# Kernel tuning notes

Hardware: AMD Instinct MI355X
Metric: run time of the kernel (lower is better)

The kernel has to match this reference:

```python
import jax, jax.numpy as jnp
import numpy as np

HID = 1024
HEADS = 16
HEAD_DIM = HID // HEADS
MAX_P = 64
TAB = 2 * MAX_P + 1
B, L = 8, 512


def setup_inputs() -> dict:
    key = jax.random.key(0)
    ks = jax.random.split(key, 16)
    def lin(k, fan_in, fan_out):
        lim = 1.0 / np.sqrt(fan_in)
        kw, kb = jax.random.split(k)
        W = jax.random.uniform(kw, (fan_out, fan_in), jnp.float32, -lim, lim)
        b = jax.random.uniform(kb, (fan_out,), jnp.float32, -lim, lim)
        return W, b
    Wq, bq = lin(ks[0], HID, HID)
    Wk, bk = lin(ks[1], HID, HID)
    Wv, bv = lin(ks[2], HID, HID)
    Wo, bo = lin(ks[3], HID, HID)
    # xavier_uniform for relative-position tables
    xlim = float(np.sqrt(6.0 / (TAB + HEAD_DIM)))
    table_k = jax.random.uniform(ks[4], (TAB, HEAD_DIM), jnp.float32, -xlim, xlim)
    table_v = jax.random.uniform(ks[5], (TAB, HEAD_DIM), jnp.float32, -xlim, xlim)
    return {
        "query": jax.random.normal(ks[6], (B, L, HID), jnp.float32),
        "key": jax.random.normal(ks[7], (B, L, HID), jnp.float32),
        "value": jax.random.normal(ks[8], (B, L, HID), jnp.float32),
        "final_mat": jax.random.randint(ks[9], (B, L, L), 0, TAB, jnp.int64 if jax.config.jax_enable_x64 else jnp.int32),
        "Wq": Wq, "bq": bq, "Wk": Wk, "bk": bk,
        "Wv": Wv, "bv": bv, "Wo": Wo, "bo": bo,
        "table_k": table_k, "table_v": table_v,
    }


def reference(query, key, value, final_mat, Wq, bq, Wk, bk, Wv, bv, Wo, bo, table_k, table_v):
    Bt, Lq, D = query.shape
    H, hd = HEADS, HEAD_DIM
    q = query @ Wq.T + bq          # [B,Lq,D]
    k = key @ Wk.T + bk            # [B,Lk,D]
    v = value @ Wv.T + bv          # [B,Lv,D]
    q4 = q.reshape(Bt, Lq, H, hd)
    k4 = k.reshape(Bt, -1, H, hd)
    v4 = v.reshape(Bt, -1, H, hd)
    # content-content scores
    attn1 = jnp.einsum('bqhd,bkhd->bhqk', q4, k4)
    # content-position scores via gathered relative-key embeddings [B,Lq,Lk,hd]
    rk = table_k[final_mat]
    attn2 = jnp.einsum('bqhd,bqkd->bhqk', q4, rk)
    scale = jnp.asarray(np.sqrt(hd), q.dtype)
    attn = jax.nn.softmax((attn1 + attn2) / scale, axis=-1)  # [B,H,Lq,Lk]
    # dropout p=0 (eval)
    w1 = jnp.einsum('bhqk,bkhd->bqhd', attn, v4)
    rv = table_v[final_mat]                                   # [B,Lq,Lk,hd]
    w2 = jnp.einsum('bhqk,bqkd->bqhd', attn, rv)
    x = (w1 + w2).reshape(Bt, Lq, D)
    return x @ Wo.T + bo
```

## Files before the change

kernel.cpp:

```cpp
#include <hip/hip_runtime.h>

#define HID 1024
#define HEADS 16
#define HD 64
#define TAB 129
#define QSTR 136
#define BATCH 8
#define SEQ 512

typedef unsigned int uint;
typedef unsigned short ushort;
typedef unsigned char uchar;
typedef __attribute__((ext_vector_type(4))) float f32x4;
typedef __attribute__((ext_vector_type(8))) __bf16 bf16x8;

__device__ __forceinline__ ushort f2b(float x) {
    uint b = __float_as_uint(x);
    uint r = (b + 0x7fffu + ((b >> 16) & 1u)) >> 16;
    return (ushort)r;
}
__device__ __forceinline__ uint pk(float lo, float hi) {
    return (uint)f2b(lo) | ((uint)f2b(hi) << 16);
}
__device__ __forceinline__ float b2f(ushort u) {
    return __uint_as_float(((uint)u) << 16);
}
union U16x8 { uint u[4]; bf16x8 v; ushort s[8]; uint4 q; };

#define GL16(gp, lp) __builtin_amdgcn_global_load_lds( \
    (const __attribute__((address_space(1))) void*)(gp), \
    (__attribute__((address_space(3))) void*)(lp), 16, 0, 0)

struct ConvArgs { const float* src[7]; ushort* dst[7]; };

__global__ __launch_bounds__(256) void convert_bf16(ConvArgs ca) {
    int bid = blockIdx.x;
    int ti, lb;
    if (bid < 6144) { ti = bid >> 11; lb = bid & 2047; }
    else { int r = bid - 6144; ti = 3 + (r >> 9); lb = r & 511; }
    const float* s = ca.src[ti] + (size_t)lb * 2048 + (threadIdx.x << 3);
    ushort*      d = ca.dst[ti] + (size_t)lb * 2048 + (threadIdx.x << 3);
    float4 a = *(const float4*)s;
    float4 c = *(const float4*)(s + 4);
    uint4 u;
    u.x = pk(a.x, a.y); u.y = pk(a.z, a.w);
    u.z = pk(c.x, c.y); u.w = pk(c.z, c.w);
    *(uint4*)d = u;
}

struct GemmArgs {
    const ushort* A[3];
    const ushort* W[3];
    const float*  bias[3];
    ushort*       Cb[3];
};

__global__ __launch_bounds__(256) void gemm_qkv(GemmArgs ga) {
    const int N = HID, K = HID;
    __shared__ ushort As[2][128 * 32];
    __shared__ ushort Bs[2][64 * 32];
    const int tid = threadIdx.x;
    const int bid = blockIdx.x;
    const int swz = (bid & 7) * 192 + (bid >> 3);
    const int z   = swz >> 9;
    const int rem = swz & 511;
    const int m0  = (rem >> 4) * 128;
    const int n0  = (rem & 15) * 64;
    const ushort* A = ga.A[z];
    const ushort* W = ga.W[z];

    const int w  = tid >> 6;
    const int l  = tid & 63;
    const int lr = l & 15;
    const int lg = l >> 4;
    const int wm = w >> 1;
    const int wn = w & 1;

    const int sr = tid >> 2;
    const int sc = tid & 3;
    const int g  = sc ^ ((sr >> 1) & 3);
    const ushort* Ag0 = A + (size_t)(m0 + sr)      * K + g * 8;
    const ushort* Ag1 = A + (size_t)(m0 + sr + 64) * K + g * 8;
    const ushort* Wg0 = W + (size_t)(n0 + sr)      * K + g * 8;

    f32x4 acc[4][2];
#pragma unroll
    for (int mt = 0; mt < 4; ++mt)
#pragma unroll
        for (int nt = 0; nt < 2; ++nt) acc[mt][nt] = (f32x4){0.f, 0.f, 0.f, 0.f};

#define STAGE(buf, k0) do { \
        GL16(Ag0 + (k0), &As[buf][w * 512]); \
        GL16(Ag1 + (k0), &As[buf][2048 + w * 512]); \
        GL16(Wg0 + (k0), &Bs[buf][w * 512]); \
    } while (0)

    const int swl = (lr >> 1) & 3;
#define COMPUTE(buf) do { \
        bf16x8 af[4], bf[2]; \
        _Pragma("unroll") \
        for (int mt = 0; mt < 4; ++mt) \
            af[mt] = *(const bf16x8*)&As[buf][(wm * 64 + mt * 16 + lr) * 32 + (lg ^ swl) * 8]; \
        _Pragma("unroll") \
        for (int nt = 0; nt < 2; ++nt) \
            bf[nt] = *(const bf16x8*)&Bs[buf][(wn * 32 + nt * 16 + lr) * 32 + (lg ^ swl) * 8]; \
        _Pragma("unroll") \
        for (int mt = 0; mt < 4; ++mt) \
            _Pragma("unroll") \
            for (int nt = 0; nt < 2; ++nt) \
                acc[mt][nt] = __builtin_amdgcn_mfma_f32_16x16x32_bf16(af[mt], bf[nt], acc[mt][nt], 0, 0, 0); \
    } while (0)

    STAGE(0, 0);
    __syncthreads();
    const int nk = K / 32;
    for (int t = 0; t < nk - 1; ++t) {
        STAGE((t + 1) & 1, (size_t)(t + 1) * 32);
        COMPUTE(t & 1);
        __syncthreads();
    }
    COMPUTE((nk - 1) & 1);

    const float* bias = ga.bias[z];
    float bv[2];
#pragma unroll
    for (int nt = 0; nt < 2; ++nt) bv[nt] = bias[n0 + wn * 32 + nt * 16 + lr];
    ushort* Cb = ga.Cb[z];
#pragma unroll
    for (int mt = 0; mt < 4; ++mt)
#pragma unroll
        for (int r4 = 0; r4 < 4; ++r4) {
            size_t m = m0 + wm * 64 + mt * 16 + lg * 4 + r4;
            ushort* crow = Cb + m * N + n0 + wn * 32 + lr;
#pragma unroll
            for (int nt = 0; nt < 2; ++nt)
                crow[nt * 16] = f2b(acc[mt][nt][r4] + bv[nt]);
        }
#undef STAGE
#undef COMPUTE
}

__global__ __launch_bounds__(256) void gemm_wo(const ushort* __restrict__ A,
                                               const ushort* __restrict__ W,
                                               const float* __restrict__ bias,
                                               float* __restrict__ Cf) {
    const int M = BATCH * SEQ, N = HID, K = HID;
    __shared__ ushort As[2][128 * 32];
    __shared__ ushort Bs[2][64 * 32];
    const int tid = threadIdx.x;
    const int m0 = blockIdx.y * 128;
    const int n0 = blockIdx.x * 64;

    const int w  = tid >> 6;
    const int l  = tid & 63;
    const int lr = l & 15;
    const int lg = l >> 4;
    const int wm = w >> 1;
    const int wn = w & 1;

    const int sr = tid >> 2;
    const int sc = tid & 3;
    const int g  = sc ^ ((sr >> 1) & 3);
    const ushort* Ag0 = A + (size_t)(m0 + sr)      * K + g * 8;
    const ushort* Ag1 = A + (size_t)(m0 + sr + 64) * K + g * 8;
    const ushort* Wg0 = W + (size_t)(n0 + sr)      * K + g * 8;

    f32x4 acc[4][2];
#pragma unroll
    for (int mt = 0; mt < 4; ++mt)
#pragma unroll
        for (int nt = 0; nt < 2; ++nt) acc[mt][nt] = (f32x4){0.f, 0.f, 0.f, 0.f};

#define STAGE(buf, k0) do { \
        GL16(Ag0 + (k0), &As[buf][w * 512]); \
        GL16(Ag1 + (k0), &As[buf][2048 + w * 512]); \
        GL16(Wg0 + (k0), &Bs[buf][w * 512]); \
    } while (0)

    const int swl = (lr >> 1) & 3;
#define COMPUTE(buf) do { \
        bf16x8 af[4], bf[2]; \
        _Pragma("unroll") \
        for (int mt = 0; mt < 4; ++mt) \
            af[mt] = *(const bf16x8*)&As[buf][(wm * 64 + mt * 16 + lr) * 32 + (lg ^ swl) * 8]; \
        _Pragma("unroll") \
        for (int nt = 0; nt < 2; ++nt) \
            bf[nt] = *(const bf16x8*)&Bs[buf][(wn * 32 + nt * 16 + lr) * 32 + (lg ^ swl) * 8]; \
        _Pragma("unroll") \
        for (int mt = 0; mt < 4; ++mt) \
            _Pragma("unroll") \
            for (int nt = 0; nt < 2; ++nt) \
                acc[mt][nt] = __builtin_amdgcn_mfma_f32_16x16x32_bf16(af[mt], bf[nt], acc[mt][nt], 0, 0, 0); \
    } while (0)

    STAGE(0, 0);
    __syncthreads();
    const int nk = K / 32;
    for (int t = 0; t < nk - 1; ++t) {
        STAGE((t + 1) & 1, (size_t)(t + 1) * 32);
        COMPUTE(t & 1);
        __syncthreads();
    }
    COMPUTE((nk - 1) & 1);

    float bv[2];
#pragma unroll
    for (int nt = 0; nt < 2; ++nt) bv[nt] = bias[n0 + wn * 32 + nt * 16 + lr];
#pragma unroll
    for (int mt = 0; mt < 4; ++mt)
#pragma unroll
        for (int r4 = 0; r4 < 4; ++r4) {
            size_t m = m0 + wm * 64 + mt * 16 + lg * 4 + r4;
            float* crow = Cf + m * N + n0 + wn * 32 + lr;
#pragma unroll
            for (int nt = 0; nt < 2; ++nt)
                crow[nt * 16] = acc[mt][nt][r4] + bv[nt];
        }
#undef STAGE
#undef COMPUTE
}

__global__ __launch_bounds__(256) void prep_kernel(const ushort* __restrict__ qb,
                                                   const float* __restrict__ table_k,
                                                   const ushort* __restrict__ vb,
                                                   const float* __restrict__ table_v,
                                                   const int* __restrict__ fmat,
                                                   ushort* __restrict__ qtab,
                                                   ushort* __restrict__ vT,
                                                   ushort* __restrict__ tvT2,
                                                   uchar* __restrict__ fm8) {
    __shared__ __align__(16) ushort shmem[144 * 72];
    const int wg  = blockIdx.x;
    const int tid = threadIdx.x;

    if (wg < 256) {
        const int h    = wg & 15;
        const int half = (wg >> 4) & 1;
        const int b    = wg >> 5;
        const int q0   = half * 256;
        ushort* tk = shmem;
        for (int i = tid; i < TAB * 8; i += 256) {
            int row = i >> 3, gr = i & 7;
            const float* src = table_k + row * HD + gr * 8;
            float4 a = *(const float4*)src;
            float4 c = *(const float4*)(src + 4);
            uint4 u;
            u.x = pk(a.x, a.y); u.y = pk(a.z, a.w);
            u.z = pk(c.x, c.y); u.w = pk(c.z, c.w);
            *(uint4*)&tk[row * 72 + gr * 8] = u;
        }
        __syncthreads();

        const int w  = tid >> 6;
        const int l  = tid & 63;
        const int lr = l & 15;
        const int lg = l >> 4;
        bf16x8 qf[4][2];
#pragma unroll
        for (int qt = 0; qt < 4; ++qt) {
            const ushort* qrow = qb + ((size_t)(b * SEQ) + q0 + w * 64 + qt * 16 + lr) * HID + h * HD;
            qf[qt][0] = *(const bf16x8*)(qrow + lg * 8);
            qf[qt][1] = *(const bf16x8*)(qrow + 32 + lg * 8);
        }
        ushort* outbase = qtab + ((size_t)(b * HEADS + h) * SEQ + q0 + w * 64) * QSTR;
#pragma unroll
        for (int mt = 0; mt < 9; ++mt) {
            bf16x8 tf0 = *(const bf16x8*)&tk[(mt * 16 + lr) * 72 + lg * 8];
            bf16x8 tf1 = *(const bf16x8*)&tk[(mt * 16 + lr) * 72 + 32 + lg * 8];
#pragma unroll
            for (int qt = 0; qt < 4; ++qt) {
                f32x4 acc = (f32x4){0.f, 0.f, 0.f, 0.f};
                acc = __builtin_amdgcn_mfma_f32_16x16x32_bf16(tf0, qf[qt][0], acc, 0, 0, 0);
                acc = __builtin_amdgcn_mfma_f32_16x16x32_bf16(tf1, qf[qt][1], acc, 0, 0, 0);
                ushort* orow = outbase + (size_t)(qt * 16 + lr) * QSTR;
                if (mt < 8) {
                    uint2 pu;
                    pu.x = pk(acc[0], acc[1]); pu.y = pk(acc[2], acc[3]);
                    *(uint2*)&orow[mt * 16 + lg * 4] = pu;
                } else if (lg == 0) {
                    orow[128] = f2b(acc[0]);
                }
            }
        }
    } else if (wg < 768) {
        const int vw = wg - 256;
        ushort* tile = shmem;
        const int b = vw >> 6, h = (vw >> 2) & 15, kc = vw & 3;
        const int k0 = kc * 128;
        {
            const int kr = tid >> 1, dc = (tid & 1) * 32;
            const ushort* src = vb + ((size_t)(b * SEQ) + k0 + kr) * HID + h * 64 + dc;
#pragma unroll
            for (int j = 0; j < 4; ++j) {
                uint4 u = *(const uint4*)(src + j * 8);
                *(uint4*)&tile[kr * 72 + dc + j * 8] = u;
            }
        }
        __syncthreads();
        {
            const int dr = tid >> 2, kc2 = (tid & 3) * 32;
            ushort* dst = vT + ((size_t)(b * 16 + h) * 64 + dr) * 512 + k0 + kc2;
#pragma unroll
            for (int j = 0; j < 4; ++j) {
                U16x8 o;
#pragma unroll
                for (int i = 0; i < 8; ++i)
                    o.s[i] = tile[(kc2 + j * 8 + i) * 72 + dr];
                *(uint4*)(dst + j * 8) = o.q;
            }
        }
    } else if (wg == 768) {
        for (int i = tid; i < 64 * 160; i += 256) {
            int d = i / 160;
            int c = i - d * 160;
            tvT2[i] = (c < TAB) ? f2b(table_v[(size_t)c * HD + d]) : (ushort)0;
        }
    } else {
        const size_t base = (size_t)(wg - 769) * 2048 + (size_t)tid * 8;
        int4 a = *(const int4*)(fmat + base);
        int4 c = *(const int4*)(fmat + base + 4);
        uint lo = (uint)a.x | ((uint)a.y << 8) | ((uint)a.z << 16) | ((uint)a.w << 24);
        uint hi = (uint)c.x | ((uint)c.y << 8) | ((uint)c.z << 16) | ((uint)c.w << 24);
        uint2 o; o.x = lo; o.y = hi;
        *(uint2*)(fm8 + base) = o;
    }
}

__global__ __launch_bounds__(256) void qk_gemm(const ushort* __restrict__ qb,
                                               const ushort* __restrict__ kb,
                                               ushort* __restrict__ S) {
    __shared__ ushort As[2][128 * 32];
    __shared__ ushort Bs[2][128 * 32];
    const int tid = threadIdx.x;
    const int m0 = blockIdx.x * 128;
    const int n0 = blockIdx.y * 128;
    const int bh = blockIdx.z;
    const int b = bh >> 4, h = bh & 15;
    const size_t rowQ = (size_t)b * SEQ;

    const int w  = tid >> 6;
    const int l  = tid & 63;
    const int lr = l & 15;
    const int lg = l >> 4;
    const int wm = w >> 1;
    const int wn = w & 1;

    const int sr = tid >> 2;
    const int sc = tid & 3;
    const int g  = sc ^ ((sr >> 1) & 3);
    const ushort* Ag0 = qb + (rowQ + m0 + sr)      * HID + h * HD + g * 8;
    const ushort* Ag1 = qb + (rowQ + m0 + sr + 64) * HID + h * HD + g * 8;
    const ushort* Wg0 = kb + (rowQ + n0 + sr)      * HID + h * HD + g * 8;
    const ushort* Wg1 = kb + (rowQ + n0 + sr + 64) * HID + h * HD + g * 8;

    GL16(Ag0,      &As[0][w * 512]); GL16(Ag1,      &As[0][2048 + w * 512]);
    GL16(Wg0,      &Bs[0][w * 512]); GL16(Wg1,      &Bs[0][2048 + w * 512]);
    GL16(Ag0 + 32, &As[1][w * 512]); GL16(Ag1 + 32, &As[1][2048 + w * 512]);
    GL16(Wg0 + 32, &Bs[1][w * 512]); GL16(Wg1 + 32, &Bs[1][2048 + w * 512]);

    f32x4 acc[4][4];
#pragma unroll
    for (int mt = 0; mt < 4; ++mt)
#pragma unroll
        for (int nt = 0; nt < 4; ++nt) acc[mt][nt] = (f32x4){0.f, 0.f, 0.f, 0.f};

    const int swl = (lr >> 1) & 3;
    __syncthreads();
#pragma unroll
    for (int buf = 0; buf < 2; ++buf) {
        bf16x8 af[4], bf[4];
#pragma unroll
        for (int mt = 0; mt < 4; ++mt)
            af[mt] = *(const bf16x8*)&As[buf][(wm * 64 + mt * 16 + lr) * 32 + (lg ^ swl) * 8];
#pragma unroll
        for (int nt = 0; nt < 4; ++nt)
            bf[nt] = *(const bf16x8*)&Bs[buf][(wn * 64 + nt * 16 + lr) * 32 + (lg ^ swl) * 8];
#pragma unroll
        for (int mt = 0; mt < 4; ++mt)
#pragma unroll
            for (int nt = 0; nt < 4; ++nt)
                acc[mt][nt] = __builtin_amdgcn_mfma_f32_16x16x32_bf16(af[mt], bf[nt], acc[mt][nt], 0, 0, 0);
    }

    ushort* Sb = S + (size_t)bh * SEQ * SEQ;
#pragma unroll
    for (int mt = 0; mt < 4; ++mt)
#pragma unroll
        for (int r4 = 0; r4 < 4; ++r4) {
            int m = m0 + wm * 64 + mt * 16 + lg * 4 + r4;
            ushort* srow = Sb + (size_t)m * SEQ + n0 + wn * 64 + lr;
#pragma unroll
            for (int nt = 0; nt < 4; ++nt)
                srow[nt * 16] = f2b(acc[mt][nt][r4]);
        }
}

__global__ __launch_bounds__(256) void sm_kernel(ushort* __restrict__ S,
                                                 const ushort* __restrict__ qt,
                                                 const uchar* __restrict__ fm8,
                                                 ushort* __restrict__ binbuf) {
    constexpr float FIX = 65536.0f;
    constexpr float INV_FIX = 1.0f / 65536.0f;
    __shared__ uint binsL[4][160];
    const int tid = threadIdx.x;
    const int wv  = tid >> 6;
    const int l   = tid & 63;
    const int gr0 = blockIdx.x * 32 + wv * 8;

    for (int ri = 0; ri < 8; ++ri) {
        const int gr = gr0 + ri;
        const int q  = gr & 511;
        const int b  = gr >> 13;
        binsL[wv][l] = 0u;
        binsL[wv][l + 64] = 0u;
        if (l < 32) binsL[wv][l + 128] = 0u;

        U16x8 sv;
        sv.q = *(const uint4*)&S[((size_t)gr << 9) + l * 8];
        const uchar* fr = fm8 + ((((size_t)b << 9) + q) << 9) + l * 8;
        uint f0 = *(const uint*)fr;
        uint f1 = *(const uint*)(fr + 4);
        const ushort* qrow = qt + (size_t)gr * QSTR;

        int ts[8];
        ts[0] = f0 & 255; ts[1] = (f0 >> 8) & 255; ts[2] = (f0 >> 16) & 255; ts[3] = f0 >> 24;
        ts[4] = f1 & 255; ts[5] = (f1 >> 8) & 255; ts[6] = (f1 >> 16) & 255; ts[7] = f1 >> 24;

        float pr[8];
        float lsum = 0.f;
#pragma unroll
        for (int j = 0; j < 8; ++j) {
            float s = b2f(sv.s[j]);
            float gv = b2f(qrow[ts[j]]);
            pr[j] = __expf((s + gv) * 0.125f);
            lsum += pr[j];
        }
#pragma unroll
        for (int j = 0; j < 8; ++j)
            __hip_atomic_fetch_add(&binsL[wv][ts[j]], (uint)(pr[j] * FIX),
                                   __ATOMIC_RELAXED, __HIP_MEMORY_SCOPE_WORKGROUP);
#pragma unroll
        for (int off = 32; off >= 1; off >>= 1)
            lsum += __shfl_xor(lsum, off);
        const float invl = 1.f / lsum;

        U16x8 pv;
#pragma unroll
        for (int j = 0; j < 4; ++j)
            pv.u[j] = pk(pr[2 * j] * invl, pr[2 * j + 1] * invl);
        *(uint4*)&S[((size_t)gr << 9) + l * 8] = pv.q;

        asm volatile("s_waitcnt lgkmcnt(0)" ::: "memory");
        ushort* bb = binbuf + (size_t)gr * 160;
        const float sc = INV_FIX * invl;
        {
            int c = 2 * l;
            *(uint*)&bb[c] = pk((float)binsL[wv][c] * sc, (float)binsL[wv][c + 1] * sc);
        }
        if (l < 16) {
            int c = 128 + 2 * l;
            *(uint*)&bb[c] = pk((float)binsL[wv][c] * sc, (float)binsL[wv][c + 1] * sc);
        }
    }
}

__global__ __launch_bounds__(256) void pv_gemm(const ushort* __restrict__ P,
                                               const ushort* __restrict__ binbuf,
                                               const ushort* __restrict__ vT,
                                               const ushort* __restrict__ tvT2,
                                               ushort* __restrict__ x) {
    __shared__ ushort As[2][128 * 32];
    __shared__ ushort Bs[2][64 * 32];
    const int tid = threadIdx.x;
    const int m0 = blockIdx.x * 128;
    const int bh = blockIdx.y;
    const int b = bh >> 4, h = bh & 15;

    const int w  = tid >> 6;
    const int l  = tid & 63;
    const int lr = l & 15;
    const int lg = l >> 4;
    const int wm = w >> 1;
    const int wn = w & 1;

    const int sr = tid >> 2;
    const int sc = tid & 3;
    const int g  = sc ^ ((sr >> 1) & 3);
    const ushort* AgS0 = P + ((size_t)bh * SEQ + m0 + sr)      * 512 + g * 8;
    const ushort* AgS1 = P + ((size_t)bh * SEQ + m0 + sr + 64) * 512 + g * 8;
    const ushort* AgB0 = binbuf + ((size_t)bh * SEQ + m0 + sr)      * 160 + g * 8;
    const ushort* AgB1 = binbuf + ((size_t)bh * SEQ + m0 + sr + 64) * 160 + g * 8;
    const ushort* WgV  = vT + ((size_t)bh * 64 + sr) * 512 + g * 8;
    const ushort* WgT  = tvT2 + (size_t)sr * 160 + g * 8;

#define STAGE_C(buf, st) do { \
        const ushort* a0_ = (st) < 16 ? AgS0 + (st) * 32 : AgB0 + ((st) - 16) * 32; \
        const ushort* a1_ = (st) < 16 ? AgS1 + (st) * 32 : AgB1 + ((st) - 16) * 32; \
        const ushort* b0_ = (st) < 16 ? WgV  + (st) * 32 : WgT  + ((st) - 16) * 32; \
        GL16(a0_, &As[buf][w * 512]); \
        GL16(a1_, &As[buf][2048 + w * 512]); \
        GL16(b0_, &Bs[buf][w * 512]); \
    } while (0)

    f32x4 acc[4][2];
#pragma unroll
    for (int mt = 0; mt < 4; ++mt)
#pragma unroll
        for (int nt = 0; nt < 2; ++nt) acc[mt][nt] = (f32x4){0.f, 0.f, 0.f, 0.f};

    const int swl = (lr >> 1) & 3;
#define COMPUTE_C(buf) do { \
        bf16x8 af[4], bf[2]; \
        _Pragma("unroll") \
        for (int mt = 0; mt < 4; ++mt) \
            af[mt] = *(const bf16x8*)&As[buf][(wm * 64 + mt * 16 + lr) * 32 + (lg ^ swl) * 8]; \
        _Pragma("unroll") \
        for (int nt = 0; nt < 2; ++nt) \
            bf[nt] = *(const bf16x8*)&Bs[buf][(wn * 32 + nt * 16 + lr) * 32 + (lg ^ swl) * 8]; \
        _Pragma("unroll") \
        for (int mt = 0; mt < 4; ++mt) \
            _Pragma("unroll") \
            for (int nt = 0; nt < 2; ++nt) \
                acc[mt][nt] = __builtin_amdgcn_mfma_f32_16x16x32_bf16(af[mt], bf[nt], acc[mt][nt], 0, 0, 0); \
    } while (0)

    STAGE_C(0, 0);
    __syncthreads();
    const int nk = 21;
    for (int t = 0; t < nk - 1; ++t) {
        STAGE_C((t + 1) & 1, t + 1);
        COMPUTE_C(t & 1);
        __syncthreads();
    }
    COMPUTE_C((nk - 1) & 1);

#pragma unroll
    for (int mt = 0; mt < 4; ++mt)
#pragma unroll
        for (int r4 = 0; r4 < 4; ++r4) {
            int m = m0 + wm * 64 + mt * 16 + lg * 4 + r4;
            ushort* orow = x + ((size_t)(b * SEQ) + m) * HID + h * HD + wn * 32 + lr;
#pragma unroll
            for (int nt = 0; nt < 2; ++nt)
                orow[nt * 16] = f2b(acc[mt][nt][r4]);
        }
#undef STAGE_C
#undef COMPUTE_C
}

extern "C" void kernel_launch(void* const* d_in, const int* in_sizes, int n_in,
                              void* d_out, int out_size, void* d_ws, size_t ws_size,
                              hipStream_t stream) {
    const float* query = (const float*)d_in[0];
    const float* key   = (const float*)d_in[1];
    const float* value = (const float*)d_in[2];
    const int*   fmat  = (const int*)d_in[3];
    const float* Wq = (const float*)d_in[4];
    const float* bq = (const float*)d_in[5];
    const float* Wk = (const float*)d_in[6];
    const float* bk = (const float*)d_in[7];
    const float* Wv = (const float*)d_in[8];
    const float* bv = (const float*)d_in[9];
    const float* Wo = (const float*)d_in[10];
    const float* bo = (const float*)d_in[11];
    const float* table_k = (const float*)d_in[12];
    const float* table_v = (const float*)d_in[13];

    const size_t nBLD = (size_t)BATCH * SEQ * HID;
    const size_t nW   = (size_t)HID * HID;
    ushort* us = (ushort*)d_ws;
    ushort* qin16 = us;                 us += nBLD;
    ushort* kin16 = us;                 us += nBLD;
    ushort* vin16 = us;                 us += nBLD;
    ushort* wq16  = us;                 us += nW;
    ushort* wk16  = us;                 us += nW;
    ushort* wv16  = us;                 us += nW;
    ushort* wo16  = us;                 us += nW;
    ushort* qb16  = us;                 us += nBLD;
    ushort* kb16  = us;                 us += nBLD;
    ushort* vb16  = us;                 us += nBLD;
    ushort* qt16  = us;                 us += (size_t)BATCH * HEADS * SEQ * QSTR;
    ushort* xb16  = us;                 us += nBLD;
    uchar*  fm8   = (uchar*)us;         us += (size_t)BATCH * SEQ * SEQ / 2;
    ushort* Sbuf  = us;                 us += (size_t)BATCH * HEADS * SEQ * SEQ;
    ushort* binbf = us;                 us += (size_t)BATCH * HEADS * SEQ * 160;

    ConvArgs ca;
    ca.src[0] = query; ca.src[1] = key; ca.src[2] = value;
    ca.src[3] = Wq; ca.src[4] = Wk; ca.src[5] = Wv; ca.src[6] = Wo;
    ca.dst[0] = qin16; ca.dst[1] = kin16; ca.dst[2] = vin16;
    ca.dst[3] = wq16; ca.dst[4] = wk16; ca.dst[5] = wv16; ca.dst[6] = wo16;
    convert_bf16<<<dim3(8192), 256, 0, stream>>>(ca);

    const int M = BATCH * SEQ;

    GemmArgs gq = {};
    gq.A[0] = qin16; gq.A[1] = kin16; gq.A[2] = vin16;
    gq.W[0] = wq16;  gq.W[1] = wk16;  gq.W[2] = wv16;
    gq.bias[0] = bq; gq.bias[1] = bk; gq.bias[2] = bv;
    gq.Cb[0] = qb16; gq.Cb[1] = kb16; gq.Cb[2] = vb16;
    gemm_qkv<<<dim3(1536), 256, 0, stream>>>(gq);

    ushort* vTbuf  = qin16;
    ushort* tvTbuf = kin16;

    prep_kernel<<<dim3(1793), 256, 0, stream>>>(qb16, table_k, vb16, table_v,
                                                fmat, qt16, vTbuf, tvTbuf, fm8);

    qk_gemm<<<dim3(4, 4, 128), 256, 0, stream>>>(qb16, kb16, Sbuf);
    sm_kernel<<<dim3(BATCH * HEADS * SEQ / 32), 256, 0, stream>>>(Sbuf, qt16, fm8, binbf);
    pv_gemm<<<dim3(4, 128), 256, 0, stream>>>(Sbuf, binbf, vTbuf, tvTbuf, xb16);

    gemm_wo<<<dim3(HID / 64, M / 128), 256, 0, stream>>>(xb16, wo16, bo, (float*)d_out);
}
```

Baseline: 178.8 us.

## Fuse softmax and PV GEMM into one kernel; enlarge QKV tiles, swizzle Wo grid

Replaces the separate softmax kernel, which wrote normalized probabilities and bin sums back to global memory, and the PV GEMM with one smpv_kernel. It computes unnormalized exp scores and feeds them straight into MFMA against V, with relative-position bins accumulated in LDS and normalization deferred to the end. It also widens the QKV GEMM tile to 128x128 (768 blocks) and adds a block swizzle to the Wo GEMM. The aim is to drop the probability write-back and reread and the binbuf round trip, at the cost of large LDS use per block and B operands loaded directly from global memory without LDS staging.

```diff
diff --git a/kernel.cpp b/kernel.cpp
--- a/kernel.cpp
+++ b/kernel.cpp
@@ -26,10 +26,22 @@
     return __uint_as_float(((uint)u) << 16);
 }
 union U16x8 { uint u[4]; bf16x8 v; ushort s[8]; uint4 q; };
+__device__ __forceinline__ bf16x8 pack8(float a0, float a1, float a2, float a3,
+                                        float a4, float a5, float a6, float a7) {
+    U16x8 r;
+    r.u[0] = pk(a0, a1); r.u[1] = pk(a2, a3);
+    r.u[2] = pk(a4, a5); r.u[3] = pk(a6, a7);
+    return r.v;
+}
 
 #define GL16(gp, lp) __builtin_amdgcn_global_load_lds( \
     (const __attribute__((address_space(1))) void*)(gp), \
     (__attribute__((address_space(3))) void*)(lp), 16, 0, 0)
+
+#define LDS_BARRIER() do { \
+        asm volatile("s_waitcnt lgkmcnt(0)" ::: "memory"); \
+        __builtin_amdgcn_s_barrier(); \
+    } while (0)
 
 struct ConvArgs { const float* src[7]; ushort* dst[7]; };
 
@@ -58,16 +70,102 @@
 __global__ __launch_bounds__(256) void gemm_qkv(GemmArgs ga) {
     const int N = HID, K = HID;
     __shared__ ushort As[2][128 * 32];
+    __shared__ ushort Bs[2][128 * 32];
+    const int tid = threadIdx.x;
+    const int bid = blockIdx.x;
+    const int swz = (bid & 7) * 96 + (bid >> 3);
+    const int z   = swz >> 8;
+    const int rem = swz & 255;
+    const int m0  = (rem >> 3) * 128;
+    const int n0  = (rem & 7) * 128;
+    const ushort* A = ga.A[z];
+    const ushort* W = ga.W[z];
+
+    const int w  = tid >> 6;
+    const int l  = tid & 63;
+    const int lr = l & 15;
+    const int lg = l >> 4;
+    const int wm = w >> 1;
+    const int wn = w & 1;
+
+    const int sr = tid >> 2;
+    const int sc = tid & 3;
+    const int g  = sc ^ ((sr >> 1) & 3);
+    const ushort* Ag0 = A + (size_t)(m0 + sr)      * K + g * 8;
+    const ushort* Ag1 = A + (size_t)(m0 + sr + 64) * K + g * 8;
+    const ushort* Wg0 = W + (size_t)(n0 + sr)      * K + g * 8;
+    const ushort* Wg1 = W + (size_t)(n0 + sr + 64) * K + g * 8;
+
+    f32x4 acc[4][4];
+#pragma unroll
+    for (int mt = 0; mt < 4; ++mt)
+#pragma unroll
+        for (int nt = 0; nt < 4; ++nt) acc[mt][nt] = (f32x4){0.f, 0.f, 0.f, 0.f};
+
+#define STAGE(buf, k0) do { \
+        GL16(Ag0 + (k0), &As[buf][w * 512]); \
+        GL16(Ag1 + (k0), &As[buf][2048 + w * 512]); \
+        GL16(Wg0 + (k0), &Bs[buf][w * 512]); \
+        GL16(Wg1 + (k0), &Bs[buf][2048 + w * 512]); \
+    } while (0)
+
+    const int swl = (lr >> 1) & 3;
+#define COMPUTE(buf) do { \
+        bf16x8 af[4], bf[4]; \
+        _Pragma("unroll") \
+        for (int mt = 0; mt < 4; ++mt) \
+            af[mt] = *(const bf16x8*)&As[buf][(wm * 64 + mt * 16 + lr) * 32 + (lg ^ swl) * 8]; \
+        _Pragma("unroll") \
+        for (int nt = 0; nt < 4; ++nt) \
+            bf[nt] = *(const bf16x8*)&Bs[buf][(wn * 64 + nt * 16 + lr) * 32 + (lg ^ swl) * 8]; \
+        _Pragma("unroll") \
+        for (int mt = 0; mt < 4; ++mt) \
+            _Pragma("unroll") \
+            for (int nt = 0; nt < 4; ++nt) \
+                acc[mt][nt] = __builtin_amdgcn_mfma_f32_16x16x32_bf16(af[mt], bf[nt], acc[mt][nt], 0, 0, 0); \
+    } while (0)
+
+    STAGE(0, 0);
+    __syncthreads();
+    const int nk = K / 32;
+    for (int t = 0; t < nk - 1; ++t) {
+        STAGE((t + 1) & 1, (size_t)(t + 1) * 32);
+        COMPUTE(t & 1);
+        __syncthreads();
+    }
+    COMPUTE((nk - 1) & 1);
+
+    const float* bias = ga.bias[z];
+    float bv[4];
+#pragma unroll
+    for (int nt = 0; nt < 4; ++nt) bv[nt] = bias[n0 + wn * 64 + nt * 16 + lr];
+    ushort* Cb = ga.Cb[z];
+#pragma unroll
+    for (int mt = 0; mt < 4; ++mt)
+#pragma unroll
+        for (int r4 = 0; r4 < 4; ++r4) {
+            size_t m = m0 + wm * 64 + mt * 16 + lg * 4 + r4;
+            ushort* crow = Cb + m * N + n0 + wn * 64 + lr;
+#pragma unroll
+            for (int nt = 0; nt < 4; ++nt)
+                crow[nt * 16] = f2b(acc[mt][nt][r4] + bv[nt]);
+        }
+#undef STAGE
+#undef COMPUTE
+}
+
+__global__ __launch_bounds__(256) void gemm_wo(const ushort* __restrict__ A,
+                                               const ushort* __restrict__ W,
+                                               const float* __restrict__ bias,
+                                               float* __restrict__ Cf) {
+    const int N = HID, K = HID;
+    __shared__ ushort As[2][128 * 32];
     __shared__ ushort Bs[2][64 * 32];
     const int tid = threadIdx.x;
     const int bid = blockIdx.x;
-    const int swz = (bid & 7) * 192 + (bid >> 3);
-    const int z   = swz >> 9;
-    const int rem = swz & 511;
-    const int m0  = (rem >> 4) * 128;
-    const int n0  = (rem & 15) * 64;
-    const ushort* A = ga.A[z];
-    const ushort* W = ga.W[z];
+    const int swz = (bid & 7) * 64 + (bid >> 3);
+    const int m0 = (swz >> 4) * 128;
+    const int n0 = (swz & 15) * 64;
 
     const int w  = tid >> 6;
     const int l  = tid & 63;
@@ -121,88 +219,6 @@
     }
     COMPUTE((nk - 1) & 1);
 
-    const float* bias = ga.bias[z];
-    float bv[2];
-#pragma unroll
-    for (int nt = 0; nt < 2; ++nt) bv[nt] = bias[n0 + wn * 32 + nt * 16 + lr];
-    ushort* Cb = ga.Cb[z];
-#pragma unroll
-    for (int mt = 0; mt < 4; ++mt)
-#pragma unroll
-        for (int r4 = 0; r4 < 4; ++r4) {
-            size_t m = m0 + wm * 64 + mt * 16 + lg * 4 + r4;
-            ushort* crow = Cb + m * N + n0 + wn * 32 + lr;
-#pragma unroll
-            for (int nt = 0; nt < 2; ++nt)
-                crow[nt * 16] = f2b(acc[mt][nt][r4] + bv[nt]);
-        }
-#undef STAGE
-#undef COMPUTE
-}
-
-__global__ __launch_bounds__(256) void gemm_wo(const ushort* __restrict__ A,
-                                               const ushort* __restrict__ W,
-                                               const float* __restrict__ bias,
-                                               float* __restrict__ Cf) {
-    const int M = BATCH * SEQ, N = HID, K = HID;
-    __shared__ ushort As[2][128 * 32];
-    __shared__ ushort Bs[2][64 * 32];
-    const int tid = threadIdx.x;
-    const int m0 = blockIdx.y * 128;
-    const int n0 = blockIdx.x * 64;
-
-    const int w  = tid >> 6;
-    const int l  = tid & 63;
-    const int lr = l & 15;
-    const int lg = l >> 4;
-    const int wm = w >> 1;
-    const int wn = w & 1;
-
-    const int sr = tid >> 2;
-    const int sc = tid & 3;
-    const int g  = sc ^ ((sr >> 1) & 3);
-    const ushort* Ag0 = A + (size_t)(m0 + sr)      * K + g * 8;
-    const ushort* Ag1 = A + (size_t)(m0 + sr + 64) * K + g * 8;
-    const ushort* Wg0 = W + (size_t)(n0 + sr)      * K + g * 8;
-
-    f32x4 acc[4][2];
-#pragma unroll
-    for (int mt = 0; mt < 4; ++mt)
-#pragma unroll
-        for (int nt = 0; nt < 2; ++nt) acc[mt][nt] = (f32x4){0.f, 0.f, 0.f, 0.f};
-
-#define STAGE(buf, k0) do { \
-        GL16(Ag0 + (k0), &As[buf][w * 512]); \
-        GL16(Ag1 + (k0), &As[buf][2048 + w * 512]); \
-        GL16(Wg0 + (k0), &Bs[buf][w * 512]); \
-    } while (0)
-
-    const int swl = (lr >> 1) & 3;
-#define COMPUTE(buf) do { \
-        bf16x8 af[4], bf[2]; \
-        _Pragma("unroll") \
-        for (int mt = 0; mt < 4; ++mt) \
-            af[mt] = *(const bf16x8*)&As[buf][(wm * 64 + mt * 16 + lr) * 32 + (lg ^ swl) * 8]; \
-        _Pragma("unroll") \
-        for (int nt = 0; nt < 2; ++nt) \
-            bf[nt] = *(const bf16x8*)&Bs[buf][(wn * 32 + nt * 16 + lr) * 32 + (lg ^ swl) * 8]; \
-        _Pragma("unroll") \
-        for (int mt = 0; mt < 4; ++mt) \
-            _Pragma("unroll") \
-            for (int nt = 0; nt < 2; ++nt) \
-                acc[mt][nt] = __builtin_amdgcn_mfma_f32_16x16x32_bf16(af[mt], bf[nt], acc[mt][nt], 0, 0, 0); \
-    } while (0)
-
-    STAGE(0, 0);
-    __syncthreads();
-    const int nk = K / 32;
-    for (int t = 0; t < nk - 1; ++t) {
-        STAGE((t + 1) & 1, (size_t)(t + 1) * 32);
-        COMPUTE(t & 1);
-        __syncthreads();
-    }
-    COMPUTE((nk - 1) & 1);
-
     float bv[2];
 #pragma unroll
     for (int nt = 0; nt < 2; ++nt) bv[nt] = bias[n0 + wn * 32 + nt * 16 + lr];
@@ -395,157 +411,124 @@
         }
 }
 
-__global__ __launch_bounds__(256) void sm_kernel(ushort* __restrict__ S,
-                                                 const ushort* __restrict__ qt,
-                                                 const uchar* __restrict__ fm8,
-                                                 ushort* __restrict__ binbuf) {
+__global__ __launch_bounds__(256) void smpv_kernel(const ushort* __restrict__ S,
+                                                   const uchar* __restrict__ fm8,
+                                                   const ushort* __restrict__ qt,
+                                                   const ushort* __restrict__ vT,
+                                                   const ushort* __restrict__ tvT2,
+                                                   ushort* __restrict__ x) {
     constexpr float FIX = 65536.0f;
     constexpr float INV_FIX = 1.0f / 65536.0f;
-    __shared__ uint binsL[4][160];
+    __shared__ __align__(16) uint   bins[64 * 132];
+    __shared__ __align__(16) ushort qtb[64 * QSTR];
+    __shared__ float rowsum[64];
+
     const int tid = threadIdx.x;
-    const int wv  = tid >> 6;
+    const int w   = tid >> 6;
     const int l   = tid & 63;
-    const int gr0 = blockIdx.x * 32 + wv * 8;
-
-    for (int ri = 0; ri < 8; ++ri) {
-        const int gr = gr0 + ri;
-        const int q  = gr & 511;
-        const int b  = gr >> 13;
-        binsL[wv][l] = 0u;
-        binsL[wv][l + 64] = 0u;
-        if (l < 32) binsL[wv][l + 128] = 0u;
-
+    const int lr  = l & 15;
+    const int lg  = l >> 4;
+
+    const int bid = blockIdx.x;
+    const int swz = (bid & 7) * 128 + (bid >> 3);
+    const int bh  = swz >> 3;
+    const int m0  = (swz & 7) * 64;
+    const int b   = bh >> 4, h = bh & 15;
+
+    {
+        const uint4* src = (const uint4*)(qt + ((size_t)bh * SEQ + m0) * QSTR);
+        uint4* dst = (uint4*)qtb;
+        for (int i = tid; i < 64 * QSTR / 8; i += 256) dst[i] = src[i];
+    }
+    {
+        uint4 z = {0u, 0u, 0u, 0u};
+        uint4* dz = (uint4*)bins;
+        for (int i = tid; i < 64 * 132 / 4; i += 256) dz[i] = z;
+    }
+    LDS_BARRIER();
+
+    const int myrow = w * 16 + lr;
+    const ushort* Srow  = S + ((size_t)bh * SEQ + m0 + myrow) * SEQ;
+    const uchar*  fmrow = fm8 + ((size_t)(b * SEQ) + m0 + myrow) * SEQ;
+    const ushort* qrow  = qtb + myrow * QSTR;
+    uint*         brow  = bins + myrow * 132;
+    const ushort* vbase = vT + (size_t)bh * 64 * 512;
+
+    f32x4 acc[4];
+#pragma unroll
+    for (int nt = 0; nt < 4; ++nt) acc[nt] = (f32x4){0.f, 0.f, 0.f, 0.f};
+    float lsum = 0.f;
+
+    for (int ks = 0; ks < 16; ++ks) {
+        const int k0 = ks * 32 + lg * 8;
         U16x8 sv;
-        sv.q = *(const uint4*)&S[((size_t)gr << 9) + l * 8];
-        const uchar* fr = fm8 + ((((size_t)b << 9) + q) << 9) + l * 8;
-        uint f0 = *(const uint*)fr;
-        uint f1 = *(const uint*)(fr + 4);
-        const ushort* qrow = qt + (size_t)gr * QSTR;
-
+        sv.q = *(const uint4*)(Srow + k0);
+        uint2 fm = *(const uint2*)(fmrow + k0);
         int ts[8];
-        ts[0] = f0 & 255; ts[1] = (f0 >> 8) & 255; ts[2] = (f0 >> 16) & 255; ts[3] = f0 >> 24;
-        ts[4] = f1 & 255; ts[5] = (f1 >> 8) & 255; ts[6] = (f1 >> 16) & 255; ts[7] = f1 >> 24;
-
-        float pr[8];
-        float lsum = 0.f;
+        ts[0] = fm.x & 255; ts[1] = (fm.x >> 8) & 255;
+        ts[2] = (fm.x >> 16) & 255; ts[3] = fm.x >> 24;
+        ts[4] = fm.y & 255; ts[5] = (fm.y >> 8) & 255;
+        ts[6] = (fm.y >> 16) & 255; ts[7] = fm.y >> 24;
+        float p[8];
 #pragma unroll
         for (int j = 0; j < 8; ++j) {
-            float s = b2f(sv.s[j]);
-            float gv = b2f(qrow[ts[j]]);
-            pr[j] = __expf((s + gv) * 0.125f);
-            lsum += pr[j];
+            p[j] = __expf((b2f(sv.s[j]) + b2f(qrow[ts[j]])) * 0.125f);
+            lsum += p[j];
         }
 #pragma unroll
         for (int j = 0; j < 8; ++j)
-            __hip_atomic_fetch_add(&binsL[wv][ts[j]], (uint)(pr[j] * FIX),
+            __hip_atomic_fetch_add(&brow[ts[j]], (uint)(p[j] * FIX),
                                    __ATOMIC_RELAXED, __HIP_MEMORY_SCOPE_WORKGROUP);
-#pragma unroll
-        for (int off = 32; off >= 1; off >>= 1)
-            lsum += __shfl_xor(lsum, off);
-        const float invl = 1.f / lsum;
-
-        U16x8 pv;
-#pragma unroll
-        for (int j = 0; j < 4; ++j)
-            pv.u[j] = pk(pr[2 * j] * invl, pr[2 * j + 1] * invl);
-        *(uint4*)&S[((size_t)gr << 9) + l * 8] = pv.q;
-
-        asm volatile("s_waitcnt lgkmcnt(0)" ::: "memory");
-        ushort* bb = binbuf + (size_t)gr * 160;
-        const float sc = INV_FIX * invl;
-        {
-            int c = 2 * l;
-            *(uint*)&bb[c] = pk((float)binsL[wv][c] * sc, (float)binsL[wv][c + 1] * sc);
-        }
-        if (l < 16) {
-            int c = 128 + 2 * l;
-            *(uint*)&bb[c] = pk((float)binsL[wv][c] * sc, (float)binsL[wv][c + 1] * sc);
-        }
-    }
-}
-
-__global__ __launch_bounds__(256) void pv_gemm(const ushort* __restrict__ P,
-                                               const ushort* __restrict__ binbuf,
-                                               const ushort* __restrict__ vT,
-                                               const ushort* __restrict__ tvT2,
-                                               ushort* __restrict__ x) {
-    __shared__ ushort As[2][128 * 32];
-    __shared__ ushort Bs[2][64 * 32];
-    const int tid = threadIdx.x;
-    const int m0 = blockIdx.x * 128;
-    const int bh = blockIdx.y;
-    const int b = bh >> 4, h = bh & 15;
-
-    const int w  = tid >> 6;
-    const int l  = tid & 63;
-    const int lr = l & 15;
-    const int lg = l >> 4;
-    const int wm = w >> 1;
-    const int wn = w & 1;
-
-    const int sr = tid >> 2;
-    const int sc = tid & 3;
-    const int g  = sc ^ ((sr >> 1) & 3);
-    const ushort* AgS0 = P + ((size_t)bh * SEQ + m0 + sr)      * 512 + g * 8;
-    const ushort* AgS1 = P + ((size_t)bh * SEQ + m0 + sr + 64) * 512 + g * 8;
-    const ushort* AgB0 = binbuf + ((size_t)bh * SEQ + m0 + sr)      * 160 + g * 8;
-    const ushort* AgB1 = binbuf + ((size_t)bh * SEQ + m0 + sr + 64) * 160 + g * 8;
-    const ushort* WgV  = vT + ((size_t)bh * 64 + sr) * 512 + g * 8;
-    const ushort* WgT  = tvT2 + (size_t)sr * 160 + g * 8;
-
-#define STAGE_C(buf, st) do { \
-        const ushort* a0_ = (st) < 16 ? AgS0 + (st) * 32 : AgB0 + ((st) - 16) * 32; \
-        const ushort* a1_ = (st) < 16 ? AgS1 + (st) * 32 : AgB1 + ((st) - 16) * 32; \
-        const ushort* b0_ = (st) < 16 ? WgV  + (st) * 32 : WgT  + ((st) - 16) * 32; \
-        GL16(a0_, &As[buf][w * 512]); \
-        GL16(a1_, &As[buf][2048 + w * 512]); \
-        GL16(b0_, &Bs[buf][w * 512]); \
-    } while (0)
-
-    f32x4 acc[4][2];
-#pragma unroll
-    for (int mt = 0; mt < 4; ++mt)
-#pragma unroll
-        for (int nt = 0; nt < 2; ++nt) acc[mt][nt] = (f32x4){0.f, 0.f, 0.f, 0.f};
-
-    const int swl = (lr >> 1) & 3;
-#define COMPUTE_C(buf) do { \
-        bf16x8 af[4], bf[2]; \
-        _Pragma("unroll") \
-        for (int mt = 0; mt < 4; ++mt) \
-            af[mt] = *(const bf16x8*)&As[buf][(wm * 64 + mt * 16 + lr) * 32 + (lg ^ swl) * 8]; \
-        _Pragma("unroll") \
-        for (int nt = 0; nt < 2; ++nt) \
-            bf[nt] = *(const bf16x8*)&Bs[buf][(wn * 32 + nt * 16 + lr) * 32 + (lg ^ swl) * 8]; \
-        _Pragma("unroll") \
-        for (int mt = 0; mt < 4; ++mt) \
-            _Pragma("unroll") \
-            for (int nt = 0; nt < 2; ++nt) \
-                acc[mt][nt] = __builtin_amdgcn_mfma_f32_16x16x32_bf16(af[mt], bf[nt], acc[mt][nt], 0, 0, 0); \
-    } while (0)
-
-    STAGE_C(0, 0);
-    __syncthreads();
-    const int nk = 21;
-    for (int t = 0; t < nk - 1; ++t) {
-        STAGE_C((t + 1) & 1, t + 1);
-        COMPUTE_C(t & 1);
-        __syncthreads();
-    }
-    COMPUTE_C((nk - 1) & 1);
-
-#pragma unroll
-    for (int mt = 0; mt < 4; ++mt)
-#pragma unroll
-        for (int r4 = 0; r4 < 4; ++r4) {
-            int m = m0 + wm * 64 + mt * 16 + lg * 4 + r4;
-            ushort* orow = x + ((size_t)(b * SEQ) + m) * HID + h * HD + wn * 32 + lr;
-#pragma unroll
-            for (int nt = 0; nt < 2; ++nt)
-                orow[nt * 16] = f2b(acc[mt][nt][r4]);
-        }
-#undef STAGE_C
-#undef COMPUTE_C
+        bf16x8 af = pack8(p[0], p[1], p[2], p[3], p[4], p[5], p[6], p[7]);
+#pragma unroll
+        for (int nt = 0; nt < 4; ++nt) {
+            bf16x8 bf_ = *(const bf16x8*)(vbase + (size_t)(nt * 16 + lr) * 512 + k0);
+            acc[nt] = __builtin_amdgcn_mfma_f32_16x16x32_bf16(af, bf_, acc[nt], 0, 0, 0);
+        }
+    }
+    lsum += __shfl_xor(lsum, 16);
+    lsum += __shfl_xor(lsum, 32);
+    if (lg == 0) rowsum[myrow] = lsum;
+
+    asm volatile("s_waitcnt lgkmcnt(0)" ::: "memory");
+
+#pragma unroll
+    for (int ks = 0; ks < 4; ++ks) {
+        const int t0 = ks * 32 + lg * 8;
+        const uint* bp = brow + t0;
+        bf16x8 af = pack8((float)bp[0] * INV_FIX, (float)bp[1] * INV_FIX,
+                          (float)bp[2] * INV_FIX, (float)bp[3] * INV_FIX,
+                          (float)bp[4] * INV_FIX, (float)bp[5] * INV_FIX,
+                          (float)bp[6] * INV_FIX, (float)bp[7] * INV_FIX);
+#pragma unroll
+        for (int nt = 0; nt < 4; ++nt) {
+            bf16x8 bf_ = *(const bf16x8*)(tvT2 + (size_t)(nt * 16 + lr) * 160 + t0);
+            acc[nt] = __builtin_amdgcn_mfma_f32_16x16x32_bf16(af, bf_, acc[nt], 0, 0, 0);
+        }
+    }
+
+    float iv[4], nb[4];
+#pragma unroll
+    for (int r = 0; r < 4; ++r) {
+        const int crow = w * 16 + lg * 4 + r;
+        iv[r] = 1.f / rowsum[crow];
+        nb[r] = (float)bins[crow * 132 + 128] * INV_FIX;
+    }
+#pragma unroll
+    for (int nt = 0; nt < 4; ++nt) {
+        float tv = b2f(tvT2[(size_t)(nt * 16 + lr) * 160 + 128]);
+#pragma unroll
+        for (int r = 0; r < 4; ++r)
+            acc[nt][r] = (acc[nt][r] + nb[r] * tv) * iv[r];
+    }
+    {
+        ushort* orow = x + ((size_t)(b * SEQ) + m0 + w * 16 + lg * 4) * HID + h * HD;
+#pragma unroll
+        for (int r = 0; r < 4; ++r)
+#pragma unroll
+            for (int nt = 0; nt < 4; ++nt)
+                orow[(size_t)r * HID + nt * 16 + lr] = f2b(acc[nt][r]);
+    }
 }
 
 extern "C" void kernel_launch(void* const* d_in, const int* in_sizes, int n_in,
@@ -583,7 +566,6 @@
     ushort* xb16  = us;                 us += nBLD;
     uchar*  fm8   = (uchar*)us;         us += (size_t)BATCH * SEQ * SEQ / 2;
     ushort* Sbuf  = us;                 us += (size_t)BATCH * HEADS * SEQ * SEQ;
-    ushort* binbf = us;                 us += (size_t)BATCH * HEADS * SEQ * 160;
 
     ConvArgs ca;
     ca.src[0] = query; ca.src[1] = key; ca.src[2] = value;
@@ -592,14 +574,12 @@
     ca.dst[3] = wq16; ca.dst[4] = wk16; ca.dst[5] = wv16; ca.dst[6] = wo16;
     convert_bf16<<<dim3(8192), 256, 0, stream>>>(ca);
 
-    const int M = BATCH * SEQ;
-
     GemmArgs gq = {};
     gq.A[0] = qin16; gq.A[1] = kin16; gq.A[2] = vin16;
     gq.W[0] = wq16;  gq.W[1] = wk16;  gq.W[2] = wv16;
     gq.bias[0] = bq; gq.bias[1] = bk; gq.bias[2] = bv;
     gq.Cb[0] = qb16; gq.Cb[1] = kb16; gq.Cb[2] = vb16;
-    gemm_qkv<<<dim3(1536), 256, 0, stream>>>(gq);
+    gemm_qkv<<<dim3(768), 256, 0, stream>>>(gq);
 
     ushort* vTbuf  = qin16;
     ushort* tvTbuf = kin16;
@@ -608,8 +588,7 @@
                                                 fmat, qt16, vTbuf, tvTbuf, fm8);
 
     qk_gemm<<<dim3(4, 4, 128), 256, 0, stream>>>(qb16, kb16, Sbuf);
-    sm_kernel<<<dim3(BATCH * HEADS * SEQ / 32), 256, 0, stream>>>(Sbuf, qt16, fm8, binbf);
-    pv_gemm<<<dim3(4, 128), 256, 0, stream>>>(Sbuf, binbf, vTbuf, tvTbuf, xb16);
-
-    gemm_wo<<<dim3(HID / 64, M / 128), 256, 0, stream>>>(xb16, wo16, bo, (float*)d_out);
-}
+    smpv_kernel<<<dim3(1024), 256, 0, stream>>>(Sbuf, fm8, qt16, vTbuf, tvTbuf, xb16);
+
+    gemm_wo<<<dim3(512), 256, 0, stream>>>(xb16, wo16, bo, (float*)d_out);
+}
```

Result: no change. 179.4 us (+0.3%).
